# Optimization experiments

Hardware: AMD Instinct MI355X
Metric: run time of the kernel (lower is better)

Reference implementation:

```python
import jax, jax.numpy as jnp
import numpy as np

ALPHA = 0.2   # LeakyReLU negative slope
NEG = -9e15   # mask fill value from the torch code


def _conv1d(x, w, b):
    # x: (N, C_in, L), w: (C_out, C_in, 5), padding=2 -> same length
    y = jax.lax.conv_general_dilated(x, w, window_strides=(1,), padding=[(2, 2)],
                                     dimension_numbers=('NCH', 'OIH', 'NCH'))
    return y + b[None, :, None]


def _gat(h, mask, W, a):
    # Faithful to a_input @ a: e_ij = leakyrelu(Wh_i . a[:H] + Wh_j . a[H:])
    Wh = jnp.einsum('bnf,fo->bno', h, W)          # (B,N,H)
    H = W.shape[1]
    f1 = Wh @ a[:H]                               # (B,N,1)
    f2 = Wh @ a[H:]                               # (B,N,1)
    e = f1 + jnp.swapaxes(f2, 1, 2)               # (B,N,N)
    e = jnp.where(e > 0, e, ALPHA * e)            # LeakyReLU
    e = jnp.where(mask, e, NEG)
    att = jax.nn.softmax(e, axis=-1)              # dropout skipped (eval mode)
    return jnp.einsum('bij,bjo->bio', att, Wh)


def setup_inputs() -> dict:
    key = jax.random.key(0)
    ks = jax.random.split(key, 14)
    B, S, N, H, E = 8, 200, 512, 64, 2048
    sc = 0.1
    return {
        'x': jax.random.normal(ks[0], (B, S, N * 2), dtype=jnp.float32),
        'adj': jax.random.randint(ks[1], (N, N), 0, 2, dtype=jnp.int32),
        'edge_index': jax.random.randint(ks[2], (E, 2), 0, N, dtype=jnp.int32),
        'conv1_w': jax.random.normal(ks[3], (H // 2, 2, 5), dtype=jnp.float32) * sc,
        'conv1_b': jnp.zeros((H // 2,), dtype=jnp.float32),
        'conv2_w': jax.random.normal(ks[4], (H, H // 2, 5), dtype=jnp.float32) * sc,
        'conv2_b': jnp.zeros((H,), dtype=jnp.float32),
        'W1': jax.random.normal(ks[5], (H, H), dtype=jnp.float32) * sc,
        'a1': jax.random.normal(ks[6], (2 * H, 1), dtype=jnp.float32) * sc,
        'W2': jax.random.normal(ks[7], (H, H), dtype=jnp.float32) * sc,
        'a2': jax.random.normal(ks[8], (2 * H, 1), dtype=jnp.float32) * sc,
        'fc1_w': jax.random.normal(ks[9], (2 * H, H), dtype=jnp.float32) * sc,
        'fc1_b': jnp.zeros((H,), dtype=jnp.float32),
        'fc2_w': jax.random.normal(ks[10], (H, 1), dtype=jnp.float32) * sc,
        'fc2_b': jnp.zeros((1,), dtype=jnp.float32),
    }


def reference(x, adj, edge_index, conv1_w, conv1_b, conv2_w, conv2_b,
              W1, a1, W2, a2, fc1_w, fc1_b, fc2_w, fc2_b):
    B = x.shape[0]
    N = adj.shape[0]
    # (B,S,2N) -> (B,N,S,2) -> (B*N,2,S)
    xn = x.reshape(B, -1, N, 2).transpose(0, 2, 1, 3)
    xf = xn.reshape(B * N, -1, 2).transpose(0, 2, 1)
    h = jax.nn.relu(_conv1d(xf, conv1_w, conv1_b))
    h = jax.nn.relu(_conv1d(h, conv2_w, conv2_b))
    h = h.mean(axis=-1)                 # AdaptiveAvgPool1d(1) + squeeze
    h = h.reshape(B, N, -1)             # (B,N,H)
    mask = (adj > 0)[None]              # (1,N,N) broadcasts over batch
    h = jax.nn.relu(_gat(h, mask, W1, a1))
    h = _gat(h, mask, W2, a2)
    h1 = h[:, edge_index[:, 0]]         # (B,E,H)
    h2 = h[:, edge_index[:, 1]]
    he = jnp.concatenate([h1, h2], axis=-1)  # (B,E,2H)
    z = jax.nn.relu(he @ fc1_w + fc1_b)
    return jax.nn.sigmoid(z @ fc2_w + fc2_b).squeeze(-1)  # (B,E)
```

## Files before the change

### kernel.cpp

```cpp
#include <hip/hip_runtime.h>
#include <hip/hip_bf16.h>

typedef unsigned short u16;
typedef __attribute__((ext_vector_type(8))) short short8;
typedef __attribute__((ext_vector_type(4))) float float4v;

#define BATCH 8
#define SLEN  200
#define NNODE 512
#define C1    32
#define C2    64
#define NEDGE 2048
#define NEGV  -9000000000000000.0f

#define H1S 40
#define H1R 212
#define A1S 32

__device__ __forceinline__ u16 f2bf(float f) {
    unsigned int x = __float_as_uint(f);
    unsigned int lsb = (x >> 16) & 1u;
    x += 0x7fffu + lsb;
    return (u16)(x >> 16);
}

__device__ __forceinline__ float bf2f(u16 u) {
    return __uint_as_float(((unsigned int)u) << 16);
}

__device__ __forceinline__ unsigned int pk2(float a, float b) {
    __hip_bfloat162 h = __float22bfloat162_rn(make_float2(a, b));
    unsigned int r;
    __builtin_memcpy(&r, &h, 4);
    return r;
}

__global__ __launch_bounds__(256) void prep_kernel(
    const float* __restrict__ w1,
    const float* __restrict__ w2,
    u16* __restrict__ w1f,
    u16* __restrict__ w2f)
{
    const int t = threadIdx.x;
    if (t < 128) {
        const int nt = t >> 6;
        const int l  = t & 63;
        const int mml = l & 15, qq = l >> 4;
        const int oc = nt * 16 + mml;
        #pragma unroll
        for (int j = 0; j < 8; ++j) {
            const int k = qq * 8 + j;
            u16 val = 0;
            if (k < 10) {
                val = f2bf(w1[oc * 10 + k]);
            } else if (k < 20) {
                val = f2bf(w1[oc * 10 + (k - 10)]);
            } else if (k < 30) {
                const float wf = w1[oc * 10 + (k - 20)];
                val = f2bf(wf - bf2f(f2bf(wf)));
            }
            w1f[(nt * 64 + l) * 8 + j] = val;
        }
    }
    const int lane = t & 63, wv = t >> 6;
    const int ml = lane & 15, q = lane >> 4;
    #pragma unroll
    for (int kk = 0; kk < 5; ++kk)
        #pragma unroll
        for (int j = 0; j < 8; ++j)
            w2f[((kk * 4 + wv) * 64 + lane) * 8 + j] =
                f2bf(w2[(size_t)(wv * 16 + ml) * 160 + (q * 8 + j) * 5 + kk]);
}

__global__ __launch_bounds__(256) void conv_fused_kernel(
    const float* __restrict__ x,
    const float* __restrict__ b1,
    const float* __restrict__ b2,
    const float* __restrict__ W1,
    const float* __restrict__ a1,
    const u16* __restrict__ w1f,
    const u16* __restrict__ w2f,
    u16* __restrict__ Wh_bt,
    float* __restrict__ f1,
    float* __restrict__ f2)
{
    __shared__ __align__(16) u16 A1[208 * A1S];
    __shared__ __align__(16) u16 h1p[H1R * H1S];
    __shared__ float hm[64];
    __shared__ float part[4][64];

    const int t    = threadIdx.x;
    const int blk  = blockIdx.x;
    const int b    = blk >> 9;
    const int n    = blk & 511;
    const int lane = t & 63;
    const int wv   = t >> 6;
    const int ml   = lane & 15;
    const int q    = lane >> 4;

    const short8 w1frag0 = *(const short8*)(w1f + lane * 8);
    const short8 w1frag1 = *(const short8*)(w1f + (64 + lane) * 8);
    short8 w2frag[5];
    #pragma unroll
    for (int kk = 0; kk < 5; ++kk)
        w2frag[kk] = *(const short8*)(w2f + ((kk * 4 + wv) * 64 + lane) * 8);
    const float bias1a = b1[ml];
    const float bias1b = b1[16 + ml];
    const float bias2  = b2[wv * 16 + ml];

    {
        const short8 z8 = {0, 0, 0, 0, 0, 0, 0, 0};
        for (int idx = t; idx < 832; idx += 256) ((short8*)A1)[idx] = z8;
        unsigned int* hz = (unsigned int*)h1p;
        if (t < 40)       hz[t] = 0u;
        else if (t < 240) hz[4040 + (t - 40)] = 0u;
    }
    __syncthreads();

    if (t < SLEN) {
        const float2 xv = *(const float2*)(x + ((size_t)(b * SLEN + t)) * (NNODE * 2) + n * 2);
        const u16 hx = f2bf(xv.x);
        const u16 hy = f2bf(xv.y);
        const u16 lx = f2bf(xv.x - bf2f(hx));
        const u16 ly = f2bf(xv.y - bf2f(hy));
        #pragma unroll
        for (int kk = 0; kk < 5; ++kk) {
            const int m = t + 2 - kk;
            if (m >= 0) {
                u16* row = &A1[m * A1S];
                row[kk]      = hx;  row[5 + kk]  = hy;
                row[10 + kk] = lx;  row[15 + kk] = ly;
                row[20 + kk] = hx;  row[25 + kk] = hy;
            }
        }
    }
    __syncthreads();

    for (int mt = wv; mt < 13; mt += 4) {
        const short8 a = *(const short8*)&A1[(mt * 16 + ml) * A1S + q * 8];
        float4v c0 = {0.f, 0.f, 0.f, 0.f};
        float4v c1 = {0.f, 0.f, 0.f, 0.f};
        c0 = __builtin_amdgcn_mfma_f32_16x16x32_bf16(a, w1frag0, c0, 0, 0, 0);
        c1 = __builtin_amdgcn_mfma_f32_16x16x32_bf16(a, w1frag1, c1, 0, 0, 0);
        #pragma unroll
        for (int r = 0; r < 4; ++r) {
            const int m = mt * 16 + q * 4 + r;
            if (m < SLEN) {
                h1p[(2 + m) * H1S + ml]      = f2bf(fmaxf(c0[r] + bias1a, 0.f));
                h1p[(2 + m) * H1S + 16 + ml] = f2bf(fmaxf(c1[r] + bias1b, 0.f));
            }
        }
    }
    __syncthreads();

    float total = 0.f;
    #pragma unroll
    for (int mt = 0; mt < 13; ++mt) {
        float4v acc = {0.f, 0.f, 0.f, 0.f};
        #pragma unroll
        for (int kk = 0; kk < 5; ++kk) {
            const short8 a = *(const short8*)&h1p[(mt * 16 + ml + kk) * H1S + q * 8];
            acc = __builtin_amdgcn_mfma_f32_16x16x32_bf16(a, w2frag[kk], acc, 0, 0, 0);
        }
        if (mt < 12) {
            #pragma unroll
            for (int r = 0; r < 4; ++r) total += fmaxf(acc[r] + bias2, 0.f);
        } else if (q < 2) {
            #pragma unroll
            for (int r = 0; r < 4; ++r) total += fmaxf(acc[r] + bias2, 0.f);
        }
    }
    total += __shfl_xor(total, 16, 64);
    total += __shfl_xor(total, 32, 64);
    if (lane < 16) hm[wv * 16 + lane] = total * (1.0f / 200.0f);
    __syncthreads();

    {
        const int o = t & 63, q4 = t >> 6;
        const float* Wp = W1 + (q4 * 16) * 64 + o;
        float p = 0.f;
        #pragma unroll
        for (int k = 0; k < 16; ++k) p += hm[q4 * 16 + k] * Wp[k * 64];
        part[q4][o] = p;
    }
    __syncthreads();
    if (t < 64) {
        const float v = part[0][t] + part[1][t] + part[2][t] + part[3][t];
        Wh_bt[((size_t)(b * 64 + t)) * 512 + n] = f2bf(v);
        float v1 = v * a1[t];
        float v2 = v * a1[64 + t];
        #pragma unroll
        for (int off = 32; off; off >>= 1) {
            v1 += __shfl_xor(v1, off, 64);
            v2 += __shfl_xor(v2, off, 64);
        }
        if (t == 0) { f1[b * 512 + n] = v1; f2[b * 512 + n] = v2; }
    }
}

__global__ __launch_bounds__(256) void gat_wh_kernel(
    const float* __restrict__ h,
    const float* __restrict__ W,
    const float* __restrict__ a,
    u16* __restrict__ Wh_bt,
    float* __restrict__ f1,
    float* __restrict__ f2)
{
    __shared__ __align__(16) u16 hA[64 * 72];
    __shared__ __align__(16) u16 Wt[64 * 72];
    __shared__ __align__(16) u16 whT[64 * 72];
    __shared__ float as[128];

    const int t    = threadIdx.x;
    const int blk  = blockIdx.x;
    const int b    = blk >> 3;
    const int j0   = (blk & 7) * 64;
    const int lane = t & 63, wv = t >> 6, ml = lane & 15, q = lane >> 4;

    {
        const int r = t >> 2, c0 = (t & 3) * 16;
        const float* hp = h + ((size_t)(b * 512 + j0 + r)) * 64 + c0;
        #pragma unroll
        for (int v = 0; v < 4; ++v) {
            float4 f = *(const float4*)(hp + v * 4);
            unsigned int* dst = (unsigned int*)&hA[r * 72 + c0 + v * 4];
            dst[0] = pk2(f.x, f.y);
            dst[1] = pk2(f.z, f.w);
        }
    }
    {
        const int k = t >> 2, o0 = (t & 3) * 16;
        const float* wp = W + k * 64 + o0;
        #pragma unroll
        for (int v = 0; v < 16; ++v)
            Wt[(o0 + v) * 72 + k] = f2bf(wp[v]);
    }
    if (t < 128) as[t] = a[t];
    __syncthreads();

    short8 af0 = *(const short8*)&hA[(16 * wv + ml) * 72 + q * 8];
    short8 af1 = *(const short8*)&hA[(16 * wv + ml) * 72 + 32 + q * 8];
    float4v acc[4];
    #pragma unroll
    for (int nt = 0; nt < 4; ++nt) {
        short8 b0 = *(const short8*)&Wt[(16 * nt + ml) * 72 + q * 8];
        short8 b1 = *(const short8*)&Wt[(16 * nt + ml) * 72 + 32 + q * 8];
        float4v c = {0.f, 0.f, 0.f, 0.f};
        c = __builtin_amdgcn_mfma_f32_16x16x32_bf16(af0, b0, c, 0, 0, 0);
        c = __builtin_amdgcn_mfma_f32_16x16x32_bf16(af1, b1, c, 0, 0, 0);
        acc[nt] = c;
    }

    #pragma unroll
    for (int nt = 0; nt < 4; ++nt) {
        unsigned int* dst = (unsigned int*)&whT[(16 * nt + ml) * 72 + 16 * wv + q * 4];
        dst[0] = pk2(acc[nt][0], acc[nt][1]);
        dst[1] = pk2(acc[nt][2], acc[nt][3]);
    }

    #pragma unroll
    for (int r = 0; r < 4; ++r) {
        float v1 = 0.f, v2 = 0.f;
        #pragma unroll
        for (int nt = 0; nt < 4; ++nt) {
            const float w = acc[nt][r];
            v1 += w * as[16 * nt + ml];
            v2 += w * as[64 + 16 * nt + ml];
        }
        v1 += __shfl_xor(v1, 1, 64); v2 += __shfl_xor(v2, 1, 64);
        v1 += __shfl_xor(v1, 2, 64); v2 += __shfl_xor(v2, 2, 64);
        v1 += __shfl_xor(v1, 4, 64); v2 += __shfl_xor(v2, 4, 64);
        v1 += __shfl_xor(v1, 8, 64); v2 += __shfl_xor(v2, 8, 64);
        if (ml == 0) {
            const int j = j0 + 16 * wv + q * 4 + r;
            f1[b * 512 + j] = v1;
            f2[b * 512 + j] = v2;
        }
    }
    __syncthreads();

    {
        const int o = t >> 2, js = (t & 3) * 16;
        u16* dst = Wh_bt + ((size_t)(b * 64 + o)) * 512 + j0 + js;
        *(short8*)dst = *(const short8*)&whT[o * 72 + js];
    }
}

#define PSTR 520
__global__ __launch_bounds__(512) void gat_attn_kernel(
    const u16* __restrict__ Wh_bt,
    const float* __restrict__ f1,
    const float* __restrict__ f2,
    const int* __restrict__ adj,
    float* __restrict__ outp,
    const int do_relu)
{
    __shared__ __align__(16) u16 P[16 * PSTR];
    __shared__ float f2s[512];
    __shared__ float invs[16];
    __shared__ float f1s[16];
    __shared__ float accH[4][64][4];

    const int t   = threadIdx.x;
    const int blk = blockIdx.x;
    const int b   = blk >> 5;
    const int i0  = (blk & 31) * 16;

    f2s[t & 511] = f2[b * 512 + (t & 511)];
    if (t < 16) f1s[t] = f1[b * 512 + i0 + t];
    __syncthreads();

    {
        const int i = t >> 5, jseg = t & 31;
        const float f1i = f1s[i];
        const int* arow = adj + (size_t)(i0 + i) * 512 + jseg * 16;
        const float* f2p = f2s + jseg * 16;
        float ev[16];
        float mx = -3.0e38f;
        #pragma unroll
        for (int v = 0; v < 4; ++v) {
            const int4 a4 = *(const int4*)(arow + v * 4);
            #pragma unroll
            for (int u = 0; u < 4; ++u) {
                const int msk = (&a4.x)[u];
                float e = f1i + f2p[v * 4 + u];
                e = e > 0.f ? e : 0.2f * e;
                e = (msk > 0) ? e : NEGV;
                ev[v * 4 + u] = e;
                mx = fmaxf(mx, e);
            }
        }
        mx = fmaxf(mx, __shfl_xor(mx, 1, 64));
        mx = fmaxf(mx, __shfl_xor(mx, 2, 64));
        mx = fmaxf(mx, __shfl_xor(mx, 4, 64));
        mx = fmaxf(mx, __shfl_xor(mx, 8, 64));
        mx = fmaxf(mx, __shfl_xor(mx, 16, 64));
        float sum = 0.f;
        #pragma unroll
        for (int v = 0; v < 16; ++v) {
            const float ex = __expf(ev[v] - mx);
            ev[v] = ex;
            sum += ex;
        }
        sum += __shfl_xor(sum, 1, 64);
        sum += __shfl_xor(sum, 2, 64);
        sum += __shfl_xor(sum, 4, 64);
        sum += __shfl_xor(sum, 8, 64);
        sum += __shfl_xor(sum, 16, 64);
        if (jseg == 0) invs[i] = 1.0f / sum;
        unsigned int* prow = (unsigned int*)&P[i * PSTR + jseg * 16];
        #pragma unroll
        for (int v = 0; v < 8; ++v)
            prow[v] = pk2(ev[2 * v], ev[2 * v + 1]);
    }
    __syncthreads();

    const int lane = t & 63, wv = t >> 6, nt = wv & 3, kh = wv >> 2;
    const int ml = lane & 15, q = lane >> 4;
    const u16* Bp = Wh_bt + ((size_t)(b * 64 + nt * 16 + ml)) * 512 + kh * 256 + q * 8;
    float4v acc = {0.f, 0.f, 0.f, 0.f};
    #pragma unroll
    for (int ks = 0; ks < 8; ++ks) {
        const short8 afr = *(const short8*)&P[ml * PSTR + kh * 256 + ks * 32 + q * 8];
        const short8 bfr = *(const short8*)(Bp + ks * 32);
        acc = __builtin_amdgcn_mfma_f32_16x16x32_bf16(afr, bfr, acc, 0, 0, 0);
    }
    if (kh == 1) {
        #pragma unroll
        for (int r = 0; r < 4; ++r) accH[nt][lane][r] = acc[r];
    }
    __syncthreads();
    if (kh == 0) {
        #pragma unroll
        for (int r = 0; r < 4; ++r) {
            const int i2 = q * 4 + r;
            float val = (acc[r] + accH[nt][lane][r]) * invs[i2];
            if (do_relu) val = fmaxf(val, 0.f);
            outp[((size_t)(b * 512 + i0 + i2)) * 64 + nt * 16 + ml] = val;
        }
    }
}

#define FSTR 136
__global__ __launch_bounds__(256) void edge_mlp_kernel(
    const float* __restrict__ hg,
    const int* __restrict__ eidx,
    const float* __restrict__ fc1w,
    const float* __restrict__ fc1b,
    const float* __restrict__ fc2w,
    const float* __restrict__ fc2b,
    float* __restrict__ out)
{
    __shared__ __align__(16) u16 fwT[64 * FSTR];
    __shared__ __align__(16) u16 he[16 * FSTR];
    __shared__ float part[16][4];
    __shared__ float b1s[64], w2s[64];

    const int t   = threadIdx.x;
    const int blk = blockIdx.x;
    const int b   = blk >> 7;
    const int e0  = (blk & 127) * 16;

    {
        const int k = t >> 1, o0 = (t & 1) * 32;
        const float* wp = fc1w + k * 64 + o0;
        #pragma unroll
        for (int v = 0; v < 32; ++v)
            fwT[(o0 + v) * FSTR + k] = f2bf(wp[v]);
    }
    if (t < 64) { b1s[t] = fc1b[t]; w2s[t] = fc2w[t]; }
    {
        const int ep = t >> 4, p = t & 15;
        const int e = e0 + ep;
        const int node = (p < 8) ? eidx[e * 2] : eidx[e * 2 + 1];
        const int c0 = (p & 7) * 8;
        const float* hp = hg + ((size_t)(b * 512 + node)) * 64 + c0;
        const float4 fa = *(const float4*)hp;
        const float4 fb = *(const float4*)(hp + 4);
        unsigned int* dst = (unsigned int*)&he[ep * FSTR + ((p < 8) ? 0 : 64) + c0];
        dst[0] = pk2(fa.x, fa.y);
        dst[1] = pk2(fa.z, fa.w);
        dst[2] = pk2(fb.x, fb.y);
        dst[3] = pk2(fb.z, fb.w);
    }
    __syncthreads();

    const int lane = t & 63, wv = t >> 6, ml = lane & 15, q = lane >> 4;
    float4v acc = {0.f, 0.f, 0.f, 0.f};
    #pragma unroll
    for (int ks = 0; ks < 4; ++ks) {
        const short8 afr = *(const short8*)&he[ml * FSTR + ks * 32 + q * 8];
        const short8 bfr = *(const short8*)&fwT[(16 * wv + ml) * FSTR + ks * 32 + q * 8];
        acc = __builtin_amdgcn_mfma_f32_16x16x32_bf16(afr, bfr, acc, 0, 0, 0);
    }
    const int o = 16 * wv + ml;
    const float bo = b1s[o], wo = w2s[o];
    #pragma unroll
    for (int r = 0; r < 4; ++r) {
        float z = fmaxf(acc[r] + bo, 0.f) * wo;
        z += __shfl_xor(z, 1, 64);
        z += __shfl_xor(z, 2, 64);
        z += __shfl_xor(z, 4, 64);
        z += __shfl_xor(z, 8, 64);
        if (ml == 0) part[q * 4 + r][wv] = z;
    }
    __syncthreads();
    if (t < 16) {
        const float v = part[t][0] + part[t][1] + part[t][2] + part[t][3] + fc2b[0];
        out[b * 2048 + e0 + t] = 1.0f / (1.0f + __expf(-v));
    }
}

extern "C" void kernel_launch(void* const* d_in, const int* in_sizes, int n_in,
                              void* d_out, int out_size, void* d_ws, size_t ws_size,
                              hipStream_t stream) {
    const float* x    = (const float*)d_in[0];
    const int* adj    = (const int*)d_in[1];
    const int* eidx   = (const int*)d_in[2];
    const float* w1   = (const float*)d_in[3];
    const float* b1   = (const float*)d_in[4];
    const float* w2   = (const float*)d_in[5];
    const float* b2   = (const float*)d_in[6];
    const float* W1   = (const float*)d_in[7];
    const float* a1   = (const float*)d_in[8];
    const float* W2   = (const float*)d_in[9];
    const float* a2   = (const float*)d_in[10];
    const float* fc1w = (const float*)d_in[11];
    const float* fc1b = (const float*)d_in[12];
    const float* fc2w = (const float*)d_in[13];
    const float* fc2b = (const float*)d_in[14];
    float* out = (float*)d_out;

    float* ws = (float*)d_ws;
    const size_t R = (size_t)BATCH * NNODE;
    float* g    = ws;
    float* f1   = g + R * 64;
    float* f2   = f1 + R;
    u16*   whbt = (u16*)(f2 + R);
    u16*   w1f  = whbt + R * 64;
    u16*   w2f  = w1f + 1024;

    prep_kernel<<<dim3(1), dim3(256), 0, stream>>>(w1, w2, w1f, w2f);
    conv_fused_kernel<<<dim3(R), dim3(256), 0, stream>>>(
        x, b1, b2, W1, a1, w1f, w2f, whbt, f1, f2);
    gat_attn_kernel<<<dim3(256), dim3(512), 0, stream>>>(whbt, f1, f2, adj, g, 1);
    gat_wh_kernel<<<dim3(64), dim3(256), 0, stream>>>(g, W2, a2, whbt, f1, f2);
    gat_attn_kernel<<<dim3(256), dim3(512), 0, stream>>>(whbt, f1, f2, adj, g, 0);
    edge_mlp_kernel<<<dim3(1024), dim3(256), 0, stream>>>(
        g, eidx, fc1w, fc1b, fc2w, fc2b, out);
}
```

Before: 156.8 us.

## Pre-transpose input and build conv1 im2col rows with packed vector stores

Adds a tiled transpose kernel so each conv block reads its node's time series contiguously instead of 8-byte strided loads across rows of x. The conv1 A-matrix is now built per row from a small packed hi/lo staging buffer and written with 16-byte stores, with the row stride padded to 40 to reduce bank conflicts. Conv1 outputs are written as packed bf16 pairs, which interleaves channels, and the conv2 weight layout is permuted to match. The cost is an extra kernel launch plus a full write and read of a transposed copy of x.

```diff
diff --git a/kernel.cpp b/kernel.cpp
--- a/kernel.cpp
+++ b/kernel.cpp
@@ -15,7 +15,7 @@
 
 #define H1S 40
 #define H1R 212
-#define A1S 32
+#define A1S 40
 
 __device__ __forceinline__ u16 f2bf(float f) {
     unsigned int x = __float_as_uint(f);
@@ -33,6 +33,33 @@
     unsigned int r;
     __builtin_memcpy(&r, &h, 4);
     return r;
+}
+
+__global__ __launch_bounds__(256) void transpose_kernel(
+    const float* __restrict__ x,
+    float* __restrict__ xT)
+{
+    __shared__ float tile[32][33];
+    const int t   = threadIdx.x;
+    const int nc0 = blockIdx.x * 32;
+    const int s0  = blockIdx.y * 32;
+    const int b   = blockIdx.z;
+    const int c   = t & 31, rr = t >> 5;
+
+    #pragma unroll
+    for (int r = 0; r < 4; ++r) {
+        const int s = s0 + rr + r * 8;
+        if (s < SLEN)
+            tile[rr + r * 8][c] = x[((size_t)(b * SLEN + s)) * 1024 + nc0 + c];
+    }
+    __syncthreads();
+    #pragma unroll
+    for (int r = 0; r < 4; ++r) {
+        const int nc = nc0 + rr + r * 8;
+        const int s = s0 + c;
+        if (s < SLEN)
+            xT[((size_t)(b * 1024 + nc)) * SLEN + s] = tile[c][rr + r * 8];
+    }
 }
 
 __global__ __launch_bounds__(256) void prep_kernel(
@@ -67,13 +94,16 @@
     #pragma unroll
     for (int kk = 0; kk < 5; ++kk)
         #pragma unroll
-        for (int j = 0; j < 8; ++j)
+        for (int j = 0; j < 8; ++j) {
+            const int c = q * 8 + j;
+            const int ic = (c & 1) * 16 + (c >> 1);
             w2f[((kk * 4 + wv) * 64 + lane) * 8 + j] =
-                f2bf(w2[(size_t)(wv * 16 + ml) * 160 + (q * 8 + j) * 5 + kk]);
+                f2bf(w2[(size_t)(wv * 16 + ml) * 160 + ic * 5 + kk]);
+        }
 }
 
 __global__ __launch_bounds__(256) void conv_fused_kernel(
-    const float* __restrict__ x,
+    const float* __restrict__ xT,
     const float* __restrict__ b1,
     const float* __restrict__ b2,
     const float* __restrict__ W1,
@@ -84,6 +114,7 @@
     float* __restrict__ f1,
     float* __restrict__ f2)
 {
+    __shared__ unsigned int xhl[2][212];
     __shared__ __align__(16) u16 A1[208 * A1S];
     __shared__ __align__(16) u16 h1p[H1R * H1S];
     __shared__ float hm[64];
@@ -108,31 +139,50 @@
     const float bias1b = b1[16 + ml];
     const float bias2  = b2[wv * 16 + ml];
 
-    {
-        const short8 z8 = {0, 0, 0, 0, 0, 0, 0, 0};
-        for (int idx = t; idx < 832; idx += 256) ((short8*)A1)[idx] = z8;
+    if (t < SLEN) {
+        const float x0 = xT[((size_t)(b * 1024 + 2 * n)) * SLEN + t];
+        const float x1 = xT[((size_t)(b * 1024 + 2 * n + 1)) * SLEN + t];
+        const u16 hx = f2bf(x0), hy = f2bf(x1);
+        const u16 lx = f2bf(x0 - bf2f(hx));
+        const u16 ly = f2bf(x1 - bf2f(hy));
+        xhl[0][2 + t] = (unsigned int)hx | ((unsigned int)lx << 16);
+        xhl[1][2 + t] = (unsigned int)hy | ((unsigned int)ly << 16);
+    } else if (t < 212) {
+        const int p = (t < 202) ? (t - 200) : t;
+        xhl[0][p] = 0u;
+        xhl[1][p] = 0u;
+    }
+    {
         unsigned int* hz = (unsigned int*)h1p;
         if (t < 40)       hz[t] = 0u;
         else if (t < 240) hz[4040 + (t - 40)] = 0u;
     }
     __syncthreads();
 
-    if (t < SLEN) {
-        const float2 xv = *(const float2*)(x + ((size_t)(b * SLEN + t)) * (NNODE * 2) + n * 2);
-        const u16 hx = f2bf(xv.x);
-        const u16 hy = f2bf(xv.y);
-        const u16 lx = f2bf(xv.x - bf2f(hx));
-        const u16 ly = f2bf(xv.y - bf2f(hy));
+    if (t < 208) {
+        unsigned int X0[5], X1[5];
         #pragma unroll
         for (int kk = 0; kk < 5; ++kk) {
-            const int m = t + 2 - kk;
-            if (m >= 0) {
-                u16* row = &A1[m * A1S];
-                row[kk]      = hx;  row[5 + kk]  = hy;
-                row[10 + kk] = lx;  row[15 + kk] = ly;
-                row[20 + kk] = hx;  row[25 + kk] = hy;
-            }
-        }
+            X0[kk] = xhl[0][t + kk];
+            X1[kk] = xhl[1][t + kk];
+        }
+        unsigned int d[16];
+        d[0] = (X0[0] & 0xffffu) | (X0[1] << 16);
+        d[1] = (X0[2] & 0xffffu) | (X0[3] << 16);
+        d[2] = (X0[4] & 0xffffu) | (X1[0] << 16);
+        d[3] = (X1[1] & 0xffffu) | (X1[2] << 16);
+        d[4] = (X1[3] & 0xffffu) | (X1[4] << 16);
+        d[5] = (X0[0] >> 16) | (X0[1] & 0xffff0000u);
+        d[6] = (X0[2] >> 16) | (X0[3] & 0xffff0000u);
+        d[7] = (X0[4] >> 16) | (X1[0] & 0xffff0000u);
+        d[8] = (X1[1] >> 16) | (X1[2] & 0xffff0000u);
+        d[9] = (X1[3] >> 16) | (X1[4] & 0xffff0000u);
+        d[10] = d[0]; d[11] = d[1]; d[12] = d[2]; d[13] = d[3]; d[14] = d[4];
+        d[15] = 0u;
+        unsigned int* row = (unsigned int*)&A1[t * A1S];
+        #pragma unroll
+        for (int ch = 0; ch < 4; ++ch)
+            *(uint4*)(row + ch * 4) = make_uint4(d[ch*4], d[ch*4+1], d[ch*4+2], d[ch*4+3]);
     }
     __syncthreads();
 
@@ -146,8 +196,8 @@
         for (int r = 0; r < 4; ++r) {
             const int m = mt * 16 + q * 4 + r;
             if (m < SLEN) {
-                h1p[(2 + m) * H1S + ml]      = f2bf(fmaxf(c0[r] + bias1a, 0.f));
-                h1p[(2 + m) * H1S + 16 + ml] = f2bf(fmaxf(c1[r] + bias1b, 0.f));
+                *(unsigned int*)&h1p[(2 + m) * H1S + 2 * ml] =
+                    pk2(fmaxf(c0[r] + bias1a, 0.f), fmaxf(c1[r] + bias1b, 0.f));
             }
         }
     }
@@ -479,10 +529,12 @@
     u16*   whbt = (u16*)(f2 + R);
     u16*   w1f  = whbt + R * 64;
     u16*   w2f  = w1f + 1024;
-
+    float* xT   = (float*)(w2f + 10240);
+
+    transpose_kernel<<<dim3(32, 7, 8), dim3(256), 0, stream>>>(x, xT);
     prep_kernel<<<dim3(1), dim3(256), 0, stream>>>(w1, w2, w1f, w2f);
     conv_fused_kernel<<<dim3(R), dim3(256), 0, stream>>>(
-        x, b1, b2, W1, a1, w1f, w2f, whbt, f1, f2);
+        xT, b1, b2, W1, a1, w1f, w2f, whbt, f1, f2);
     gat_attn_kernel<<<dim3(256), dim3(512), 0, stream>>>(whbt, f1, f2, adj, g, 1);
     gat_wh_kernel<<<dim3(64), dim3(256), 0, stream>>>(g, W2, a2, whbt, f1, f2);
     gat_attn_kernel<<<dim3(256), dim3(512), 0, stream>>>(whbt, f1, f2, adj, g, 0);
```

Measured after the change: 142.6 us. 1.1x faster.

## Pre-transpose x, compute conv1 in fp32 VALU, prepack fc1 weights

Applied to the files above, without the earlier changes.

Adds a transpose pass inside the prep kernel so each conv block reads its node's time series contiguously instead of striding across 1024-wide rows. Conv1 now runs as fp32 scalar FMAs rather than a bf16 hi/lo split MFMA, and its output channels are interleaved to match a permuted w2 fragment packing. Conv2 is split across waves by output-channel pair and half of the time tiles, then reduced through shared memory. The edge MLP loads prepacked bf16 fc1 fragments instead of transposing fc1 per block. The cost is an extra full read and write of x through global memory, in exchange for coalesced loads in the conv kernel.

```diff
diff --git a/kernel.cpp b/kernel.cpp
--- a/kernel.cpp
+++ b/kernel.cpp
@@ -8,14 +8,11 @@
 #define BATCH 8
 #define SLEN  200
 #define NNODE 512
-#define C1    32
-#define C2    64
 #define NEDGE 2048
 #define NEGV  -9000000000000000.0f
 
 #define H1S 40
 #define H1R 212
-#define A1S 32
 
 __device__ __forceinline__ u16 f2bf(float f) {
     unsigned int x = __float_as_uint(f);
@@ -35,57 +32,82 @@
     return r;
 }
 
-__global__ __launch_bounds__(256) void prep_kernel(
-    const float* __restrict__ w1,
+__global__ __launch_bounds__(256) void pre_kernel(
+    const float* __restrict__ x,
     const float* __restrict__ w2,
-    u16* __restrict__ w1f,
-    u16* __restrict__ w2f)
+    const float* __restrict__ fc1w,
+    float* __restrict__ xT,
+    u16* __restrict__ w2f,
+    u16* __restrict__ efw)
 {
+    __shared__ float tile[32][33];
     const int t = threadIdx.x;
-    if (t < 128) {
-        const int nt = t >> 6;
-        const int l  = t & 63;
-        const int mml = l & 15, qq = l >> 4;
-        const int oc = nt * 16 + mml;
-        #pragma unroll
-        for (int j = 0; j < 8; ++j) {
-            const int k = qq * 8 + j;
-            u16 val = 0;
-            if (k < 10) {
-                val = f2bf(w1[oc * 10 + k]);
-            } else if (k < 20) {
-                val = f2bf(w1[oc * 10 + (k - 10)]);
-            } else if (k < 30) {
-                const float wf = w1[oc * 10 + (k - 20)];
-                val = f2bf(wf - bf2f(f2bf(wf)));
-            }
-            w1f[(nt * 64 + l) * 8 + j] = val;
-        }
-    }
+    const int blk = blockIdx.x;
+
+    if (blk < 1792) {
+        const int xi  = blk & 31;
+        const int rem = blk >> 5;
+        const int yi  = rem % 7;
+        const int zi  = rem / 7;
+        const int nc0 = xi * 32;
+        const int s0  = yi * 32;
+        const int c   = t & 31, rr = t >> 5;
+        #pragma unroll
+        for (int r = 0; r < 4; ++r) {
+            const int s = s0 + rr + r * 8;
+            if (s < SLEN)
+                tile[rr + r * 8][c] = x[((size_t)(zi * SLEN + s)) * 1024 + nc0 + c];
+        }
+        __syncthreads();
+        #pragma unroll
+        for (int r = 0; r < 4; ++r) {
+            const int nc = nc0 + rr + r * 8;
+            const int s = s0 + c;
+            if (s < SLEN)
+                xT[((size_t)(zi * 1024 + nc)) * SLEN + s] = tile[c][rr + r * 8];
+        }
+        return;
+    }
+
     const int lane = t & 63, wv = t >> 6;
     const int ml = lane & 15, q = lane >> 4;
-    #pragma unroll
-    for (int kk = 0; kk < 5; ++kk)
-        #pragma unroll
-        for (int j = 0; j < 8; ++j)
-            w2f[((kk * 4 + wv) * 64 + lane) * 8 + j] =
-                f2bf(w2[(size_t)(wv * 16 + ml) * 160 + (q * 8 + j) * 5 + kk]);
+
+    for (int fid = wv; fid < 20; fid += 4) {
+        const int kk = fid >> 2, ot = fid & 3;
+        const int oc = ot * 16 + ml;
+        #pragma unroll
+        for (int j = 0; j < 8; ++j) {
+            const int c  = q * 8 + j;
+            const int ic = (c & 1) * 16 + (c >> 1);
+            w2f[(fid * 64 + lane) * 8 + j] = f2bf(w2[(size_t)oc * 160 + ic * 5 + kk]);
+        }
+    }
+    for (int u = wv; u < 16; u += 4) {
+        const int ks = u >> 2, wvv = u & 3;
+        const int o = wvv * 16 + ml;
+        #pragma unroll
+        for (int j = 0; j < 8; ++j) {
+            const int k = ks * 32 + q * 8 + j;
+            efw[(u * 64 + lane) * 8 + j] = f2bf(fc1w[k * 64 + o]);
+        }
+    }
 }
 
 __global__ __launch_bounds__(256) void conv_fused_kernel(
-    const float* __restrict__ x,
+    const float* __restrict__ xT,
+    const float* __restrict__ w1,
     const float* __restrict__ b1,
     const float* __restrict__ b2,
     const float* __restrict__ W1,
     const float* __restrict__ a1,
-    const u16* __restrict__ w1f,
     const u16* __restrict__ w2f,
     u16* __restrict__ Wh_bt,
     float* __restrict__ f1,
     float* __restrict__ f2)
 {
-    __shared__ __align__(16) u16 A1[208 * A1S];
+    __shared__ float xs[2][212];
     __shared__ __align__(16) u16 h1p[H1R * H1S];
+    __shared__ float red[4][32];
     __shared__ float hm[64];
     __shared__ float part[4][64];
 
@@ -98,90 +120,117 @@
     const int ml   = lane & 15;
     const int q    = lane >> 4;
 
-    const short8 w1frag0 = *(const short8*)(w1f + lane * 8);
-    const short8 w1frag1 = *(const short8*)(w1f + (64 + lane) * 8);
-    short8 w2frag[5];
-    #pragma unroll
-    for (int kk = 0; kk < 5; ++kk)
-        w2frag[kk] = *(const short8*)(w2f + ((kk * 4 + wv) * 64 + lane) * 8);
-    const float bias1a = b1[ml];
-    const float bias1b = b1[16 + ml];
-    const float bias2  = b2[wv * 16 + ml];
-
-    {
-        const short8 z8 = {0, 0, 0, 0, 0, 0, 0, 0};
-        for (int idx = t; idx < 832; idx += 256) ((short8*)A1)[idx] = z8;
+    const int p = t & 15;
+    const int g = t >> 4;
+
+    const int o2 = wv & 1;
+    const int mh = wv >> 1;
+
+    short8 wfA[5], wfB[5];
+    #pragma unroll
+    for (int kk = 0; kk < 5; ++kk) {
+        wfA[kk] = *(const short8*)(w2f + ((kk * 4 + o2 * 2 + 0) * 64 + lane) * 8);
+        wfB[kk] = *(const short8*)(w2f + ((kk * 4 + o2 * 2 + 1) * 64 + lane) * 8);
+    }
+    const float bias2a = b2[o2 * 32 + ml];
+    const float bias2b = b2[o2 * 32 + 16 + ml];
+
+    float wA[10], wB[10];
+    #pragma unroll
+    for (int j = 0; j < 10; ++j) {
+        wA[j] = w1[p * 10 + j];
+        wB[j] = w1[(16 + p) * 10 + j];
+    }
+    const float b1a = b1[p], b1b = b1[16 + p];
+
+    if (t < SLEN) {
+        const float* xp = xT + ((size_t)(b * 1024 + 2 * n)) * SLEN + t;
+        xs[0][2 + t] = xp[0];
+        xs[1][2 + t] = xp[SLEN];
+    } else if (t < 212) {
+        const int pp = (t < 202) ? (t - 200) : t;
+        xs[0][pp] = 0.f;
+        xs[1][pp] = 0.f;
+    }
+    {
         unsigned int* hz = (unsigned int*)h1p;
         if (t < 40)       hz[t] = 0u;
-        else if (t < 240) hz[4040 + (t - 40)] = 0u;
-    }
-    __syncthreads();
-
-    if (t < SLEN) {
-        const float2 xv = *(const float2*)(x + ((size_t)(b * SLEN + t)) * (NNODE * 2) + n * 2);
-        const u16 hx = f2bf(xv.x);
-        const u16 hy = f2bf(xv.y);
-        const u16 lx = f2bf(xv.x - bf2f(hx));
-        const u16 ly = f2bf(xv.y - bf2f(hy));
-        #pragma unroll
-        for (int kk = 0; kk < 5; ++kk) {
-            const int m = t + 2 - kk;
-            if (m >= 0) {
-                u16* row = &A1[m * A1S];
-                row[kk]      = hx;  row[5 + kk]  = hy;
-                row[10 + kk] = lx;  row[15 + kk] = ly;
-                row[20 + kk] = hx;  row[25 + kk] = hy;
+        else if (t < 240) hz[4000 + t] = 0u;
+    }
+    __syncthreads();
+
+    #pragma unroll
+    for (int u = 0; u < 4; ++u) {
+        const int base = 4 * g + 64 * u;
+        if (base < SLEN) {
+            float X0[8], X1[8];
+            *(float4*)&X0[0] = *(const float4*)&xs[0][base];
+            *(float4*)&X0[4] = *(const float4*)&xs[0][base + 4];
+            *(float4*)&X1[0] = *(const float4*)&xs[1][base];
+            *(float4*)&X1[4] = *(const float4*)&xs[1][base + 4];
+            #pragma unroll
+            for (int i = 0; i < 4; ++i) {
+                float a0 = b1a, a1 = b1b;
+                #pragma unroll
+                for (int k = 0; k < 5; ++k) {
+                    const float x0 = X0[i + k], x1 = X1[i + k];
+                    a0 += wA[k] * x0 + wA[5 + k] * x1;
+                    a1 += wB[k] * x0 + wB[5 + k] * x1;
+                }
+                *(unsigned int*)&h1p[(2 + base + i) * H1S + 2 * p] =
+                    pk2(fmaxf(a0, 0.f), fmaxf(a1, 0.f));
             }
         }
     }
     __syncthreads();
 
-    for (int mt = wv; mt < 13; mt += 4) {
-        const short8 a = *(const short8*)&A1[(mt * 16 + ml) * A1S + q * 8];
-        float4v c0 = {0.f, 0.f, 0.f, 0.f};
-        float4v c1 = {0.f, 0.f, 0.f, 0.f};
-        c0 = __builtin_amdgcn_mfma_f32_16x16x32_bf16(a, w1frag0, c0, 0, 0, 0);
-        c1 = __builtin_amdgcn_mfma_f32_16x16x32_bf16(a, w1frag1, c1, 0, 0, 0);
-        #pragma unroll
-        for (int r = 0; r < 4; ++r) {
-            const int m = mt * 16 + q * 4 + r;
-            if (m < SLEN) {
-                h1p[(2 + m) * H1S + ml]      = f2bf(fmaxf(c0[r] + bias1a, 0.f));
-                h1p[(2 + m) * H1S + 16 + ml] = f2bf(fmaxf(c1[r] + bias1b, 0.f));
-            }
-        }
-    }
-    __syncthreads();
-
-    float total = 0.f;
-    #pragma unroll
-    for (int mt = 0; mt < 13; ++mt) {
-        float4v acc = {0.f, 0.f, 0.f, 0.f};
+    float tA = 0.f, tB = 0.f;
+    const int mt0 = mh * 7, mtE = mh ? 13 : 7;
+    for (int mt = mt0; mt < mtE; ++mt) {
+        float4v acc0 = {0.f, 0.f, 0.f, 0.f};
+        float4v acc1 = {0.f, 0.f, 0.f, 0.f};
         #pragma unroll
         for (int kk = 0; kk < 5; ++kk) {
             const short8 a = *(const short8*)&h1p[(mt * 16 + ml + kk) * H1S + q * 8];
-            acc = __builtin_amdgcn_mfma_f32_16x16x32_bf16(a, w2frag[kk], acc, 0, 0, 0);
+            acc0 = __builtin_amdgcn_mfma_f32_16x16x32_bf16(a, wfA[kk], acc0, 0, 0, 0);
+            acc1 = __builtin_amdgcn_mfma_f32_16x16x32_bf16(a, wfB[kk], acc1, 0, 0, 0);
         }
         if (mt < 12) {
             #pragma unroll
-            for (int r = 0; r < 4; ++r) total += fmaxf(acc[r] + bias2, 0.f);
+            for (int r = 0; r < 4; ++r) {
+                tA += fmaxf(acc0[r] + bias2a, 0.f);
+                tB += fmaxf(acc1[r] + bias2b, 0.f);
+            }
         } else if (q < 2) {
             #pragma unroll
-            for (int r = 0; r < 4; ++r) total += fmaxf(acc[r] + bias2, 0.f);
-        }
-    }
-    total += __shfl_xor(total, 16, 64);
-    total += __shfl_xor(total, 32, 64);
-    if (lane < 16) hm[wv * 16 + lane] = total * (1.0f / 200.0f);
+            for (int r = 0; r < 4; ++r) {
+                tA += fmaxf(acc0[r] + bias2a, 0.f);
+                tB += fmaxf(acc1[r] + bias2b, 0.f);
+            }
+        }
+    }
+    tA += __shfl_xor(tA, 16, 64);
+    tA += __shfl_xor(tA, 32, 64);
+    tB += __shfl_xor(tB, 16, 64);
+    tB += __shfl_xor(tB, 32, 64);
+    if (lane < 16) {
+        red[wv][ml]      = tA;
+        red[wv][16 + ml] = tB;
+    }
+    __syncthreads();
+    if (t < 64) {
+        const int grp = t >> 5, idx = t & 31;
+        hm[t] = (red[grp][idx] + red[grp + 2][idx]) * (1.0f / 200.0f);
+    }
     __syncthreads();
 
     {
         const int o = t & 63, q4 = t >> 6;
         const float* Wp = W1 + (q4 * 16) * 64 + o;
-        float p = 0.f;
-        #pragma unroll
-        for (int k = 0; k < 16; ++k) p += hm[q4 * 16 + k] * Wp[k * 64];
-        part[q4][o] = p;
+        float pv = 0.f;
+        #pragma unroll
+        for (int k = 0; k < 16; ++k) pv += hm[q4 * 16 + k] * Wp[k * 64];
+        part[q4][o] = pv;
     }
     __syncthreads();
     if (t < 64) {
@@ -385,30 +434,29 @@
 __global__ __launch_bounds__(256) void edge_mlp_kernel(
     const float* __restrict__ hg,
     const int* __restrict__ eidx,
-    const float* __restrict__ fc1w,
+    const u16* __restrict__ efw,
     const float* __restrict__ fc1b,
     const float* __restrict__ fc2w,
     const float* __restrict__ fc2b,
     float* __restrict__ out)
 {
-    __shared__ __align__(16) u16 fwT[64 * FSTR];
     __shared__ __align__(16) u16 he[16 * FSTR];
     __shared__ float part[16][4];
-    __shared__ float b1s[64], w2s[64];
 
     const int t   = threadIdx.x;
     const int blk = blockIdx.x;
     const int b   = blk >> 7;
     const int e0  = (blk & 127) * 16;
-
-    {
-        const int k = t >> 1, o0 = (t & 1) * 32;
-        const float* wp = fc1w + k * 64 + o0;
-        #pragma unroll
-        for (int v = 0; v < 32; ++v)
-            fwT[(o0 + v) * FSTR + k] = f2bf(wp[v]);
-    }
-    if (t < 64) { b1s[t] = fc1b[t]; w2s[t] = fc2w[t]; }
+    const int lane = t & 63, wv = t >> 6, ml = lane & 15, q = lane >> 4;
+
+    short8 bw[4];
+    #pragma unroll
+    for (int ks = 0; ks < 4; ++ks)
+        bw[ks] = *(const short8*)(efw + ((ks * 4 + wv) * 64 + lane) * 8);
+    const int o = 16 * wv + ml;
+    const float bo = fc1b[o];
+    const float wo = fc2w[o];
+
     {
         const int ep = t >> 4, p = t & 15;
         const int e = e0 + ep;
@@ -425,16 +473,12 @@
     }
     __syncthreads();
 
-    const int lane = t & 63, wv = t >> 6, ml = lane & 15, q = lane >> 4;
     float4v acc = {0.f, 0.f, 0.f, 0.f};
     #pragma unroll
     for (int ks = 0; ks < 4; ++ks) {
         const short8 afr = *(const short8*)&he[ml * FSTR + ks * 32 + q * 8];
-        const short8 bfr = *(const short8*)&fwT[(16 * wv + ml) * FSTR + ks * 32 + q * 8];
-        acc = __builtin_amdgcn_mfma_f32_16x16x32_bf16(afr, bfr, acc, 0, 0, 0);
-    }
-    const int o = 16 * wv + ml;
-    const float bo = b1s[o], wo = w2s[o];
+        acc = __builtin_amdgcn_mfma_f32_16x16x32_bf16(afr, bw[ks], acc, 0, 0, 0);
+    }
     #pragma unroll
     for (int r = 0; r < 4; ++r) {
         float z = fmaxf(acc[r] + bo, 0.f) * wo;
@@ -477,15 +521,16 @@
     float* f1   = g + R * 64;
     float* f2   = f1 + R;
     u16*   whbt = (u16*)(f2 + R);
-    u16*   w1f  = whbt + R * 64;
-    u16*   w2f  = w1f + 1024;
-
-    prep_kernel<<<dim3(1), dim3(256), 0, stream>>>(w1, w2, w1f, w2f);
-    conv_fused_kernel<<<dim3(R), dim3(256), 0, stream>>>(
-        x, b1, b2, W1, a1, w1f, w2f, whbt, f1, f2);
+    u16*   w2f  = whbt + R * 64;
+    u16*   efw  = w2f + 10240;
+    float* xT   = (float*)(efw + 8192);
+
+    pre_kernel<<<dim3(1793), dim3(256), 0, stream>>>(x, w2, fc1w, xT, w2f, efw);
+    conv_fused_kernel<<<dim3(4096), dim3(256), 0, stream>>>(
+        xT, w1, b1, b2, W1, a1, w2f, whbt, f1, f2);
     gat_attn_kernel<<<dim3(256), dim3(512), 0, stream>>>(whbt, f1, f2, adj, g, 1);
     gat_wh_kernel<<<dim3(64), dim3(256), 0, stream>>>(g, W2, a2, whbt, f1, f2);
     gat_attn_kernel<<<dim3(256), dim3(512), 0, stream>>>(whbt, f1, f2, adj, g, 0);
     edge_mlp_kernel<<<dim3(1024), dim3(256), 0, stream>>>(
-        g, eidx, fc1w, fc1b, fc2w, fc2b, out);
-}
+        g, eidx, efw, fc1b, fc2w, fc2b, out);
+}
```

New measurement: 142.5 us. 9.1% less time.
